# Kernel tuning notes

Hardware: AMD Instinct MI355X
Metric: run time of the kernel (lower is better)

## Reference

```python
import jax, jax.numpy as jnp
import numpy as np

# bitsandbytes NF4 codebook (16 levels)
NF4_CODE = jnp.array([
    -1.0, -0.6961928009986877, -0.5250730514526367, -0.39491748809814453,
    -0.28444138169288635, -0.18477343022823334, -0.09105003625154495, 0.0,
    0.07958029955625534, 0.16093020141124725, 0.24611230194568634,
    0.33791524171829224, 0.44070982933044434, 0.5626170039176941,
    0.7229568362236023, 1.0], dtype=jnp.float32)

L, D, KV, F, V = 2, 4096, 1024, 14336, 32000   # layers, d_model, kv_dim, ffn, vocab
H, HK, HD = 32, 8, 128                          # q heads, kv heads, head dim
B, S = 2, 1024
BLK = 64                                        # NF4 quant blocksize
ROPE_THETA = 500000.0
RMS_EPS = 1e-5


def _dequant(idx, absmax, shape):
    # idx: uint8 flat codes in [0,16); absmax: fp32 per-64-element block scale
    w = NF4_CODE[idx.astype(jnp.int32)]
    return (w.reshape(-1, BLK) * absmax[:, None]).reshape(shape)


def _rmsnorm(x, w):
    return x * jax.lax.rsqrt(jnp.mean(x * x, axis=-1, keepdims=True) + RMS_EPS) * w


def _rope(x, cos, sin):
    d2 = x.shape[-1] // 2
    x1, x2 = x[..., :d2], x[..., d2:]
    return jnp.concatenate([x1 * cos - x2 * sin, x2 * cos + x1 * sin], axis=-1)


def setup_inputs() -> dict:
    key = jax.random.key(0)
    ks = iter(jax.random.split(key, 64))

    def idx(n):
        return jax.random.randint(next(ks), (n,), 0, 16).astype(jnp.uint8)

    def amax(n):
        return jax.random.uniform(next(ks), (n // BLK,), minval=0.01, maxval=0.05)

    def qw(n):
        return (jnp.stack([idx(n) for _ in range(L)]),
                jnp.stack([amax(n) for _ in range(L)]))

    inp = {}
    inp["input_ids"] = jax.random.randint(next(ks), (B, S), 0, V, dtype=jnp.int32)
    inp["attention_mask"] = jnp.ones((B, S), dtype=jnp.int32)
    inp["embed"] = jax.random.normal(next(ks), (V, D), dtype=jnp.float32) * 0.02
    inp["q_idx"], inp["q_absmax"] = qw(D * D)
    inp["k_idx"], inp["k_absmax"] = qw(KV * D)
    inp["v_idx"], inp["v_absmax"] = qw(KV * D)
    inp["o_idx"], inp["o_absmax"] = qw(D * D)
    inp["gate_idx"], inp["gate_absmax"] = qw(F * D)
    inp["up_idx"], inp["up_absmax"] = qw(F * D)
    inp["down_idx"], inp["down_absmax"] = qw(D * F)
    inp["ln1_w"] = jnp.ones((L, D), dtype=jnp.float32)
    inp["ln2_w"] = jnp.ones((L, D), dtype=jnp.float32)
    inp["final_ln_w"] = jnp.ones((D,), dtype=jnp.float32)
    return inp


def reference(input_ids, attention_mask, embed,
              q_idx, q_absmax, k_idx, k_absmax, v_idx, v_absmax,
              o_idx, o_absmax, gate_idx, gate_absmax, up_idx, up_absmax,
              down_idx, down_absmax, ln1_w, ln2_w, final_ln_w):
    b, s = input_ids.shape
    h = embed[input_ids]                                  # [B,S,D]
    pos = jnp.arange(s, dtype=jnp.float32)
    inv = 1.0 / (ROPE_THETA ** (jnp.arange(0, HD, 2, dtype=jnp.float32) / HD))
    ang = pos[:, None] * inv[None, :]                     # [S,HD/2]
    cos = jnp.cos(ang)[None, :, None, :]
    sin = jnp.sin(ang)[None, :, None, :]
    causal = jnp.tril(jnp.ones((s, s), dtype=bool))
    mask = causal[None, None] & (attention_mask[:, None, None, :] > 0)  # [B,1,S,S]
    neg = jnp.finfo(h.dtype).min

    for l in range(L):
        x = _rmsnorm(h, ln1_w[l])
        q = x @ _dequant(q_idx[l], q_absmax[l], (D, D)).T
        k = x @ _dequant(k_idx[l], k_absmax[l], (KV, D)).T
        v = x @ _dequant(v_idx[l], v_absmax[l], (KV, D)).T
        q = _rope(q.reshape(b, s, H, HD), cos, sin)
        k = _rope(k.reshape(b, s, HK, HD), cos, sin)
        v = v.reshape(b, s, HK, HD)
        k = jnp.repeat(k, H // HK, axis=2)                # GQA expand
        v = jnp.repeat(v, H // HK, axis=2)
        scores = jnp.einsum('bqhd,bkhd->bhqk', q, k) / np.float32(np.sqrt(HD))
        scores = jnp.where(mask, scores, neg)
        attn = jax.nn.softmax(scores, axis=-1)
        ctx = jnp.einsum('bhqk,bkhd->bqhd', attn, v).reshape(b, s, D)
        h = h + ctx @ _dequant(o_idx[l], o_absmax[l], (D, D)).T
        x = _rmsnorm(h, ln2_w[l])
        g = x @ _dequant(gate_idx[l], gate_absmax[l], (F, D)).T
        u = x @ _dequant(up_idx[l], up_absmax[l], (F, D)).T
        h = h + (jax.nn.silu(g) * u) @ _dequant(down_idx[l], down_absmax[l], (D, F)).T

    h = _rmsnorm(h, final_ln_w)                           # last hidden state
    m = attention_mask.astype(h.dtype)[..., None]         # masked mean pool
    pooled = (h * m).sum(axis=1) / jnp.clip(m.sum(axis=1), 1e-9)
    return pooled
```

## Files before the change

kernel.cpp:

```cpp
#include <hip/hip_runtime.h>
#include <hip/hip_fp16.h>
#include <cstdint>
#include <cstddef>

#define B_  2
#define S_  1024
#define D_  4096
#define KV_ 1024
#define F_  14336
#define H_  32
#define HK_ 8
#define HD_ 128
#define M_  2048

typedef _Float16 f16;
typedef f16   f16x8 __attribute__((ext_vector_type(8)));
typedef f16   f16x4 __attribute__((ext_vector_type(4)));
typedef float f32x4 __attribute__((ext_vector_type(4)));

#define AS1(p) ((const __attribute__((address_space(1))) void*)(p))
#define AS3(p) ((__attribute__((address_space(3))) void*)(p))

__device__ __constant__ float NF4_C[16] = {
 -1.0f, -0.6961928009986877f, -0.5250730514526367f, -0.39491748809814453f,
 -0.28444138169288635f, -0.18477343022823334f, -0.09105003625154495f, 0.0f,
 0.07958029955625534f, 0.16093020141124725f, 0.24611230194568634f,
 0.33791524171829224f, 0.44070982933044434f, 0.5626170039176941f,
 0.7229568362236023f, 1.0f };

__global__ void k_detect(const unsigned* __restrict__ p, int* __restrict__ flag){
    if (threadIdx.x == 0){
        int u8 = 0;
        for (int i = 0; i < 256; ++i) if (p[i] >= 16u) { u8 = 1; break; }
        *flag = u8;
    }
}

__global__ __launch_bounds__(256) void k_dequant(const void* __restrict__ idxBase, size_t elemOff,
        const float* __restrict__ amax, f16* __restrict__ out, const int* __restrict__ flag)
{
    __shared__ __half2 T[3856];
    int t = threadIdx.x;
    if (t < 256){
        int b0 = t & 15, b1 = t >> 4;
        T[b0 + (b1 << 8)] = __halves2half2(__float2half(NF4_C[b0]), __float2half(NF4_C[b1]));
    }
    __syncthreads();
    size_t i = ((size_t)blockIdx.x * 256 + t) * 16;
    float am = amax[i >> 6];
    __half2 am2 = __float2half2_rn(am);
    union { __half2 h2[8]; uint4 u4[2]; } R;
    if (*flag){
        uint4 u = *(const uint4*)((const uint8_t*)idxBase + elemOff + i);
        unsigned w[4] = {u.x, u.y, u.z, u.w};
        #pragma unroll
        for (int j = 0; j < 4; ++j){
            R.h2[j*2+0] = __hmul2(T[w[j] & 0xFFFFu], am2);
            R.h2[j*2+1] = __hmul2(T[w[j] >> 16],     am2);
        }
    } else {
        const int4* s4 = (const int4*)((const int*)idxBase + elemOff + i);
        #pragma unroll
        for (int j = 0; j < 4; ++j){
            int4 a = s4[j];
            R.h2[j*2+0] = __hmul2(T[a.x | (a.y << 8)], am2);
            R.h2[j*2+1] = __hmul2(T[a.z | (a.w << 8)], am2);
        }
    }
    uint4* o = (uint4*)(out + i);
    o[0] = R.u4[0]; o[1] = R.u4[1];
}

__global__ __launch_bounds__(256) void k_embed(const int* __restrict__ ids,
        const float* __restrict__ E, float* __restrict__ Hh)
{
    int row = blockIdx.x, t = threadIdx.x;
    int id = ids[row];
    const float4* s4 = (const float4*)(E + (size_t)id * D_);
    float4* d4 = (float4*)(Hh + (size_t)row * D_);
    #pragma unroll
    for (int i = 0; i < 4; ++i) d4[t + 256*i] = s4[t + 256*i];
}

__global__ __launch_bounds__(256) void k_ropetab(float* __restrict__ cosT, float* __restrict__ sinT){
    int id = blockIdx.x * 256 + threadIdx.x;
    int d = id & 63, s = id >> 6;
    float inv = powf(500000.0f, -(float)d * (1.0f/64.0f));
    float ang = (float)s * inv;
    cosT[id] = cosf(ang);
    sinT[id] = sinf(ang);
}

__global__ void k_maskadd(const int* __restrict__ am, float* __restrict__ ma){
    int i = blockIdx.x * 256 + threadIdx.x;
    ma[i] = am[i] ? 0.f : -1e30f;
}

template<int F16OUT>
__global__ __launch_bounds__(256) void k_rmsnorm(const float* __restrict__ X,
        const float* __restrict__ W, void* __restrict__ outv)
{
    int row = blockIdx.x, t = threadIdx.x;
    const float4* x4 = (const float4*)(X + (size_t)row * D_);
    float4 xs[4]; float ss = 0.f;
    #pragma unroll
    for (int i = 0; i < 4; ++i){
        xs[i] = x4[t + 256*i];
        ss += xs[i].x*xs[i].x + xs[i].y*xs[i].y + xs[i].z*xs[i].z + xs[i].w*xs[i].w;
    }
    for (int m = 32; m; m >>= 1) ss += __shfl_xor(ss, m, 64);
    __shared__ float red[4];
    if ((t & 63) == 0) red[t >> 6] = ss;
    __syncthreads();
    ss = red[0] + red[1] + red[2] + red[3];
    float rs = rsqrtf(ss * (1.0f / D_) + 1e-5f);
    #pragma unroll
    for (int i = 0; i < 4; ++i){
        int c0 = (t + 256*i) * 4;
        float4 wv = *(const float4*)(W + c0);
        float o0 = xs[i].x*rs*wv.x, o1 = xs[i].y*rs*wv.y;
        float o2 = xs[i].z*rs*wv.z, o3 = xs[i].w*rs*wv.w;
        if (F16OUT){
            f16x4 ov = { (f16)o0, (f16)o1, (f16)o2, (f16)o3 };
            *(f16x4*)((f16*)outv + (size_t)row * D_ + c0) = ov;
        } else {
            float4 ov = {o0, o1, o2, o3};
            *(float4*)((float*)outv + (size_t)row * D_ + c0) = ov;
        }
    }
}

template<int LNH>
__global__ __launch_bounds__(256) void k_rope(const f16* __restrict__ in, int istr,
        f16* __restrict__ outp, const float* __restrict__ cosT, const float* __restrict__ sinT)
{
    int p = blockIdx.x * 256 + threadIdx.x;
    int d = p & 63;
    int h = (p >> 6) & ((1 << LNH) - 1);
    int s = (p >> (6 + LNH)) & (S_ - 1);
    int b = p >> (16 + LNH);
    size_t ib = (size_t)(b * S_ + s) * istr + (size_t)h * HD_;
    float x1 = (float)in[ib + d], x2 = (float)in[ib + 64 + d];
    float c = cosT[s*64 + d], sn = sinT[s*64 + d];
    size_t ob = (((size_t)((b << LNH) + h)) * S_ + (size_t)s) * HD_;
    outp[ob + d]      = (f16)(x1 * c - x2 * sn);
    outp[ob + 64 + d] = (f16)(x2 * c + x1 * sn);
}

__global__ __launch_bounds__(256) void k_vtrans(const f16* __restrict__ in, int istr,
        f16* __restrict__ outp){
    int p = blockIdx.x * 256 + threadIdx.x;
    int s  = p & (S_ - 1);
    int d  = (p >> 10) & (HD_ - 1);
    int hk = (p >> 17) & (HK_ - 1);
    int b  = p >> 20;
    f16 v = in[(size_t)(b * S_ + s) * istr + (size_t)hk * HD_ + d];
    outp[(((size_t)(b * HK_ + hk)) * HD_ + d) * S_ + s] = v;
}

__global__ __launch_bounds__(256) void k_flash(const f16* __restrict__ Qr, const f16* __restrict__ Kr,
        const f16* __restrict__ Vt, const float* __restrict__ mAddG, f16* __restrict__ ctx)
{
    __shared__ f16 KS[8192];
    __shared__ f16 VS[8192];
    __shared__ f16 PS[8192];
    const int t = threadIdx.x;
    const int w = t >> 6, l = t & 63;
    const int lr = l & 15, lg = l >> 4;
    const int qt = blockIdx.x, bh = blockIdx.y;
    const int b = bh >> 5, hh = bh & 31, hk = hh >> 2;
    const f16* Qb = Qr + ((size_t)bh * S_ + (size_t)qt*128) * HD_;
    const f16* Kb = Kr + (size_t)(b * HK_ + hk) * S_ * HD_;
    const f16* Vb = Vt + (size_t)(b * HK_ + hk) * HD_ * S_;

    auto stage16x128 = [&](const f16* src, int lds_, f16* dst){
        int rowl = t >> 4;
        int cs = ((t & 15) ^ (rowl & 7)) << 3;
        #pragma unroll
        for (int g = 0; g < 4; ++g)
            __builtin_amdgcn_global_load_lds(AS1(src + (size_t)(g*16 + rowl)*lds_ + cs),
                AS3(dst + g*2048 + w*512), 16, 0, 0);
    };
    auto stage32x64 = [&](const f16* src, int lds_, f16* dst){
        int rowl = t >> 3;
        int cs = ((t & 7) ^ (rowl & 7)) << 3;
        #pragma unroll
        for (int g = 0; g < 4; ++g)
            __builtin_amdgcn_global_load_lds(AS1(src + (size_t)(g*32 + rowl)*lds_ + cs),
                AS3(dst + g*2048 + w*512), 16, 0, 0);
    };

    stage16x128(Qb, HD_, KS);
    stage16x128(Qb + 64*HD_, HD_, VS);
    __syncthreads();
    f16x8 qF[2][4];
    {
        const f16* qsrc = (w < 2) ? KS : VS;
        int rbase = (w & 1) * 32;
        #pragma unroll
        for (int m = 0; m < 2; ++m)
            #pragma unroll
            for (int kd = 0; kd < 4; ++kd){
                int row = rbase + m*16 + lr;
                qF[m][kd] = *(const f16x8*)&qsrc[row*128 + (((kd*4 + lg) ^ (row & 7)) << 3)];
            }
    }
    __syncthreads();

    float mrow[2][4], lrow[2][4];
    f32x4 oacc[2][8];
    #pragma unroll
    for (int m = 0; m < 2; ++m)
        #pragma unroll
        for (int r = 0; r < 4; ++r){ mrow[m][r] = -1e30f; lrow[m][r] = 0.f; }
    #pragma unroll
    for (int m = 0; m < 2; ++m)
        #pragma unroll
        for (int dn = 0; dn < 8; ++dn){ f32x4 z = {0,0,0,0}; oacc[m][dn] = z; }

    const float ISQ = 0.08838834764831845f;
    const int ktMax = 2*qt + 1;

    for (int kt = 0; kt <= ktMax; ++kt){
        stage16x128(Kb + (size_t)(kt*64)*HD_, HD_, KS);
        __syncthreads();

        f32x4 sacc[2][4];
        #pragma unroll
        for (int m = 0; m < 2; ++m)
            #pragma unroll
            for (int n = 0; n < 4; ++n){ f32x4 z = {0,0,0,0}; sacc[m][n] = z; }
        #pragma unroll
        for (int n = 0; n < 4; ++n){
            int krow = n*16 + lr;
            #pragma unroll
            for (int kd = 0; kd < 4; ++kd){
                f16x8 kF = *(const f16x8*)&KS[krow*128 + (((kd*4 + lg) ^ (krow & 7)) << 3)];
                #pragma unroll
                for (int m = 0; m < 2; ++m)
                    sacc[m][n] = __builtin_amdgcn_mfma_f32_16x16x32_f16(qF[m][kd], kF, sacc[m][n], 0, 0, 0);
            }
        }

        stage32x64(Vb + kt*64, S_, VS);

        float mAdd[4];
        #pragma unroll
        for (int n = 0; n < 4; ++n) mAdd[n] = mAddG[b*S_ + kt*64 + n*16 + lr];
        int diag = (kt >= 2*qt);
        #pragma unroll
        for (int m = 0; m < 2; ++m)
        #pragma unroll
        for (int n = 0; n < 4; ++n)
        #pragma unroll
        for (int r = 0; r < 4; ++r){
            float s = sacc[m][n][r] * ISQ + mAdd[n];
            if (diag && (kt*64 + n*16 + lr) > (qt*128 + w*32 + m*16 + lg*4 + r)) s = -1e30f;
            sacc[m][n][r] = s;
        }
        #pragma unroll
        for (int m = 0; m < 2; ++m)
        #pragma unroll
        for (int r = 0; r < 4; ++r){
            float tm = fmaxf(fmaxf(sacc[m][0][r], sacc[m][1][r]), fmaxf(sacc[m][2][r], sacc[m][3][r]));
            #pragma unroll
            for (int msk = 1; msk < 16; msk <<= 1) tm = fmaxf(tm, __shfl_xor(tm, msk, 64));
            float mn = fmaxf(mrow[m][r], tm);
            float scl = __expf(mrow[m][r] - mn);
            mrow[m][r] = mn;
            float rs = 0.f;
            #pragma unroll
            for (int n = 0; n < 4; ++n){
                float p = __expf(sacc[m][n][r] - mn);
                sacc[m][n][r] = p; rs += p;
            }
            #pragma unroll
            for (int msk = 1; msk < 16; msk <<= 1) rs += __shfl_xor(rs, msk, 64);
            lrow[m][r] = lrow[m][r] * scl + rs;
            #pragma unroll
            for (int dn = 0; dn < 8; ++dn) oacc[m][dn][r] *= scl;
        }
        #pragma unroll
        for (int m = 0; m < 2; ++m)
        #pragma unroll
        for (int n = 0; n < 4; ++n)
        #pragma unroll
        for (int r = 0; r < 4; ++r){
            int rowl = m*16 + lg*4 + r;
            int slot = (n*2 + (lr >> 3)) ^ (rowl & 7);
            PS[w*2048 + rowl*64 + slot*8 + (lr & 7)] = (f16)sacc[m][n][r];
        }
        __syncthreads();

        f16x8 pF[2][2];
        #pragma unroll
        for (int m = 0; m < 2; ++m)
            #pragma unroll
            for (int kd = 0; kd < 2; ++kd){
                int prow = m*16 + lr;
                pF[m][kd] = *(const f16x8*)&PS[w*2048 + prow*64 + (((kd*4 + lg) ^ (prow & 7)) << 3)];
            }
        #pragma unroll
        for (int dn = 0; dn < 8; ++dn){
            int vrow = dn*16 + lr;
            #pragma unroll
            for (int kd = 0; kd < 2; ++kd){
                f16x8 vF = *(const f16x8*)&VS[vrow*64 + (((kd*4 + lg) ^ (vrow & 7)) << 3)];
                #pragma unroll
                for (int m = 0; m < 2; ++m)
                    oacc[m][dn] = __builtin_amdgcn_mfma_f32_16x16x32_f16(pF[m][kd], vF, oacc[m][dn], 0, 0, 0);
            }
        }
        __syncthreads();
    }

    #pragma unroll
    for (int m = 0; m < 2; ++m)
    #pragma unroll
    for (int dn = 0; dn < 8; ++dn)
    #pragma unroll
    for (int r = 0; r < 4; ++r){
        int grow = qt*128 + w*32 + m*16 + lg*4 + r;
        int gcol = hh*128 + dn*16 + lr;
        float v = oacc[m][dn][r] / fmaxf(lrow[m][r], 1e-30f);
        ctx[((size_t)(b * S_) + grow) * D_ + gcol] = (f16)v;
    }
}

template<int OUT>
__global__ __launch_bounds__(512, 1) void k_gemm3(const f16* __restrict__ A, const f16* __restrict__ Bp,
        void* __restrict__ Cv, const f16* __restrict__ G, int Kd, int ldk, int ldc)
{
    __shared__ f16 LDS[65536];
    const int t = threadIdx.x;
    const int w = t >> 6, l = t & 63;
    const int wm = w >> 2, wn = w & 3;

    int gx = gridDim.x, gy = gridDim.y;
    int nWG = gx * gy * gridDim.z;
    int n = (blockIdx.z * gy + blockIdx.y) * gx + blockIdx.x;
    int q = nWG >> 3;
    int sw = (n & 7) * q + (n >> 3);
    int bx = sw % gx; int r1 = sw / gx; int by = r1 % gy; int bz = r1 / gy;

    const int row0 = by * 256, col0 = bx * 256;
    const size_t koff = (size_t)bz * Kd;
    const int NT = Kd >> 6;

    const int swzk = ((t & 7) ^ ((t >> 3) & 7)) * 8;
    const f16* pA[2]; const f16* pB[2];
    #pragma unroll
    for (int l2 = 0; l2 < 2; ++l2){
        pA[l2] = A  + (size_t)(row0 + l2*128 + (t >> 3)) * ldk + koff + swzk;
        int wnc = (l2*64 + (t >> 3)) >> 5;
        pB[l2] = Bp + (size_t)(col0 + wnc*64 + ((t >> 3) & 31)) * ldk + koff + swzk;
    }

    auto stA = [&](int g, int tt, int buf){
        size_t so = (size_t)tt * 64;
        #pragma unroll
        for (int l2 = 0; l2 < 2; ++l2)
            __builtin_amdgcn_global_load_lds(AS1(pA[l2] + (size_t)g*64*ldk + so),
                AS3(&LDS[buf*16384 + g*8192 + l2*4096 + w*512]), 16, 0, 0);
    };
    auto stB = [&](int g, int tt, int buf){
        size_t so = (size_t)tt * 64;
        #pragma unroll
        for (int l2 = 0; l2 < 2; ++l2)
            __builtin_amdgcn_global_load_lds(AS1(pB[l2] + (size_t)g*32*ldk + so),
                AS3(&LDS[32768 + buf*16384 + g*8192 + l2*4096 + w*512]), 16, 0, 0);
    };

    const int lrow = (l & 15) * 64;
    const int kp0 = (((l >> 4))     ^ (l & 7)) * 8;
    const int kp1 = ((4 + (l >> 4)) ^ (l & 7)) * 8;

    f16x8 aR[2][4], bR0[2][2], bR1[2][2];
    auto rdA = [&](int g, int buf){
        int base = buf*16384 + g*8192 + wm*4096 + lrow;
        #pragma unroll
        for (int mf = 0; mf < 4; ++mf){
            aR[0][mf] = *(const f16x8*)&LDS[base + mf*1024 + kp0];
            aR[1][mf] = *(const f16x8*)&LDS[base + mf*1024 + kp1];
        }
    };
    auto rdB = [&](int g, int buf, f16x8 (&bR)[2][2]){
        int base = 32768 + buf*16384 + g*8192 + wn*2048 + lrow;
        #pragma unroll
        for (int nf = 0; nf < 2; ++nf){
            bR[0][nf] = *(const f16x8*)&LDS[base + nf*1024 + kp0];
            bR[1][nf] = *(const f16x8*)&LDS[base + nf*1024 + kp1];
        }
    };

    f32x4 zero = {0.f, 0.f, 0.f, 0.f};
    f32x4 acc[8][4];
    #pragma unroll
    for (int mi = 0; mi < 8; ++mi)
        #pragma unroll
        for (int ni = 0; ni < 4; ++ni) acc[mi][ni] = zero;

    #define MMQ(qm, qn, bR) { \
        __builtin_amdgcn_s_setprio(1); \
        _Pragma("unroll") \
        for (int ks = 0; ks < 2; ++ks) \
            _Pragma("unroll") \
            for (int mf = 0; mf < 4; ++mf) \
                _Pragma("unroll") \
                for (int nf = 0; nf < 2; ++nf) \
                    acc[(qm)*4+mf][(qn)*2+nf] = __builtin_amdgcn_mfma_f32_16x16x32_f16(aR[ks][mf], bR[ks][nf], acc[(qm)*4+mf][(qn)*2+nf], 0, 0, 0); \
        __builtin_amdgcn_s_setprio(0); }
    #define LGKM0 { asm volatile("s_waitcnt lgkmcnt(0)" ::: "memory"); __builtin_amdgcn_sched_barrier(0); }
    #define VM4   { asm volatile("s_waitcnt vmcnt(4)" ::: "memory"); }
    #define BAR   __builtin_amdgcn_s_barrier()

    stA(0, 0, 0); stB(1, 0, 0); stA(1, 0, 0); stB(0, 0, 0);
    if (NT > 1){ stA(0, 1, 1); stB(1, 1, 1); }
    VM4; BAR;

    for (int tt = 0; tt < NT; tt += 2){
        int c2 = (tt + 2 < NT) ? tt + 2 : NT - 1;
        int c3 = (tt + 3 < NT) ? tt + 3 : NT - 1;
        rdA(0, 0); rdB(0, 0, bR0);
        stA(1, tt+1 < NT ? tt+1 : NT-1, 1); stB(0, tt+1 < NT ? tt+1 : NT-1, 1);
        BAR; LGKM0; MMQ(0, 0, bR0); BAR;
        rdB(1, 0, bR1);
        BAR; LGKM0; MMQ(0, 1, bR1); BAR;
        rdA(1, 0);
        stA(0, c2, 0);
        BAR; LGKM0; MMQ(1, 1, bR1); BAR;
        stB(1, c2, 0);
        BAR; MMQ(1, 0, bR0); VM4; BAR;
        rdA(0, 1); rdB(0, 1, bR0);
        stA(1, c2, 0); stB(0, c2, 0);
        BAR; LGKM0; MMQ(0, 0, bR0); BAR;
        rdB(1, 1, bR1);
        BAR; LGKM0; MMQ(0, 1, bR1); BAR;
        rdA(1, 1);
        stA(0, c3, 1);
        BAR; LGKM0; MMQ(1, 1, bR1); BAR;
        stB(1, c3, 1);
        BAR; MMQ(1, 0, bR0); VM4; BAR;
    }

    #pragma unroll
    for (int mi = 0; mi < 8; ++mi)
    #pragma unroll
    for (int ni = 0; ni < 4; ++ni)
    #pragma unroll
    for (int r = 0; r < 4; ++r){
        int row = row0 + wm*128 + mi*16 + ((l >> 4) << 2) + r;
        int col = col0 + wn*64  + ni*16 + (l & 15);
        float v = acc[mi][ni][r];
        if (OUT == 0){
            ((float*)Cv)[(size_t)bz * ((size_t)M_ * ldc) + (size_t)row * ldc + col] = v;
        } else if (OUT == 2){
            ((f16*)Cv)[(size_t)row * ldc + col] = (f16)v;
        } else {
            size_t idx = (size_t)row * ldc + col;
            float g = (float)G[idx];
            float sg = g / (1.f + __expf(-g));
            ((f16*)Cv)[idx] = (f16)(sg * v);
        }
    }
    #undef MMQ
    #undef LGKM0
    #undef VM4
    #undef BAR
}

__global__ __launch_bounds__(256) void k_comb(const float* __restrict__ p0, const float* __restrict__ p1,
        float* __restrict__ outv)
{
    size_t i = ((size_t)blockIdx.x * 256 + threadIdx.x) * 4;
    float4 a = *(const float4*)(p0 + i);
    float4 b = *(const float4*)(p1 + i);
    float4 hv = *(const float4*)(outv + i);
    hv.x += a.x + b.x; hv.y += a.y + b.y; hv.z += a.z + b.z; hv.w += a.w + b.w;
    *(float4*)(outv + i) = hv;
}

__global__ __launch_bounds__(256) void k_pool1(const float* __restrict__ Hn, const int* __restrict__ amask,
        float* __restrict__ part, float* __restrict__ cntp)
{
    int d0 = blockIdx.x * 256 + threadIdx.x;
    int b  = blockIdx.y;
    int z  = blockIdx.z;
    int s0 = z * 128;
    float s = 0.f;
    for (int i = 0; i < 128; ++i){
        int row = s0 + i;
        if (amask[b * S_ + row])
            s += Hn[((size_t)(b * S_ + row)) * D_ + d0];
    }
    part[((size_t)(z * B_ + b)) * D_ + d0] = s;
    if (blockIdx.x == 0 && threadIdx.x == 0){
        float c = 0.f;
        for (int i = 0; i < 128; ++i) c += (amask[b * S_ + s0 + i] != 0) ? 1.f : 0.f;
        cntp[z * B_ + b] = c;
    }
}
__global__ __launch_bounds__(256) void k_pool2(const float* __restrict__ part, const float* __restrict__ cntp,
        float* __restrict__ outp)
{
    int gid = blockIdx.x * 256 + threadIdx.x;
    int b = gid >> 12, d = gid & (D_ - 1);
    float s = 0.f, c = 0.f;
    #pragma unroll
    for (int z = 0; z < 8; ++z){
        s += part[((size_t)(z * B_ + b)) * D_ + d];
        c += cntp[z * B_ + b];
    }
    outp[gid] = s / fmaxf(c, 1e-9f);
}

extern "C" void kernel_launch(void* const* d_in, const int* in_sizes, int n_in,
                              void* d_out, int out_size, void* d_ws, size_t ws_size,
                              hipStream_t stream)
{
    (void)in_sizes; (void)n_in; (void)out_size; (void)ws_size;
    const int*   ids   = (const int*)  d_in[0];
    const int*   amask = (const int*)  d_in[1];
    const float* embed = (const float*)d_in[2];
    const void*  qi = d_in[3];  const float* qa = (const float*)d_in[4];
    const void*  ki = d_in[5];  const float* ka = (const float*)d_in[6];
    const void*  vi = d_in[7];  const float* va = (const float*)d_in[8];
    const void*  oi = d_in[9];  const float* oa = (const float*)d_in[10];
    const void*  gi = d_in[11]; const float* ga = (const float*)d_in[12];
    const void*  ui = d_in[13]; const float* ua = (const float*)d_in[14];
    const void*  di = d_in[15]; const float* da = (const float*)d_in[16];
    const float* ln1 = (const float*)d_in[17];
    const float* ln2 = (const float*)d_in[18];
    const float* lnf = (const float*)d_in[19];

    const size_t DD  = (size_t)D_ * D_;
    const size_t KVD = (size_t)KV_ * D_;
    const size_t FD  = (size_t)F_ * D_;

    char* ws = (char*)d_ws;
    int*   flag = (int*)ws;
    float* h    = (float*)(ws + 256);
    float* cosT = (float*)(ws + 256 + 33554432);
    float* sinT = cosT + 65536;
    f16*   xin  = (f16*)(ws + 34078976);
    f16*   wbuf = (f16*)(ws + 50856192);
    char*  R4   = ws + 168296704;
    f16* qkv16 = (f16*)(R4);
    f16* qr  = (f16*)(R4 + 25165824);
    f16* kr  = (f16*)(R4 + 41943040);
    f16* vtr = (f16*)(R4 + 46137344);
    f16* ctx = (f16*)(R4 + 50331648);
    char* R5 = R4 + 67108864;
    f16*    gbuf   = (f16*)R5;
    float*  pR5_0  = (float*)R5;
    float*  pR5_1  = (float*)(R5 + 33554432);
    float*  pR4_0  = (float*)R4;
    float*  pR4_1  = (float*)(R4 + 33554432);
    float*  hn     = (float*)R4;
    float*  part   = (float*)R5;
    float*  cntp   = (float*)(R5 + 1048576);
    float*  maskAdd= (float*)(ws + 310378496);

    const int QKV_N = D_ + 2 * KV_;

    k_detect <<<1, 64, 0, stream>>>((const unsigned*)qi, flag);
    k_embed  <<<M_, 256, 0, stream>>>(ids, embed, h);
    k_ropetab<<<256, 256, 0, stream>>>(cosT, sinT);
    k_maskadd<<<(B_*S_)/256, 256, 0, stream>>>(amask, maskAdd);

    for (int l = 0; l < 2; ++l){
        size_t oDD = (size_t)l * DD, oKVD = (size_t)l * KVD, oFD = (size_t)l * FD;
        k_rmsnorm<1><<<M_, 256, 0, stream>>>(h, ln1 + l * D_, xin);

        k_dequant<<<DD / 4096, 256, 0, stream>>>(qi, oDD, qa + oDD/64, wbuf, flag);
        k_dequant<<<KVD / 4096, 256, 0, stream>>>(ki, oKVD, ka + oKVD/64, wbuf + DD, flag);
        k_dequant<<<KVD / 4096, 256, 0, stream>>>(vi, oKVD, va + oKVD/64, wbuf + DD + KVD, flag);
        k_gemm3<2><<<dim3(QKV_N/256, M_/256, 1), 512, 0, stream>>>(xin, wbuf, qkv16, nullptr, D_, D_, QKV_N);

        k_rope<5><<<(B_*S_*H_*64)/256, 256, 0, stream>>>(qkv16, QKV_N, qr, cosT, sinT);
        k_rope<3><<<(B_*S_*HK_*64)/256, 256, 0, stream>>>(qkv16 + D_, QKV_N, kr, cosT, sinT);
        k_vtrans <<<(B_*HK_*HD_*S_)/256, 256, 0, stream>>>(qkv16 + D_ + KV_, QKV_N, vtr);

        k_flash<<<dim3(S_/128, B_*H_), 256, 0, stream>>>(qr, kr, vtr, maskAdd, ctx);

        k_dequant<<<DD / 4096, 256, 0, stream>>>(oi, oDD, oa + oDD/64, wbuf, flag);
        k_gemm3<0><<<dim3(D_/256, M_/256, 2), 512, 0, stream>>>(ctx, wbuf, pR5_0, nullptr, D_/2, D_, D_);
        k_comb<<<(M_*D_)/1024, 256, 0, stream>>>(pR5_0, pR5_1, h);

        k_rmsnorm<1><<<M_, 256, 0, stream>>>(h, ln2 + l * D_, xin);
        k_dequant<<<FD / 4096, 256, 0, stream>>>(gi, oFD, ga + oFD/64, wbuf, flag);
        k_gemm3<2><<<dim3(F_/256, M_/256, 1), 512, 0, stream>>>(xin, wbuf, gbuf, nullptr, D_, D_, F_);
        k_dequant<<<FD / 4096, 256, 0, stream>>>(ui, oFD, ua + oFD/64, wbuf, flag);
        k_gemm3<3><<<dim3(F_/256, M_/256, 1), 512, 0, stream>>>(xin, wbuf, gbuf, gbuf, D_, D_, F_);
        k_dequant<<<FD / 4096, 256, 0, stream>>>(di, oFD, da + oFD/64, wbuf, flag);
        k_gemm3<0><<<dim3(D_/256, M_/256, 2), 512, 0, stream>>>(gbuf, wbuf, pR4_0, nullptr, F_/2, F_, D_);
        k_comb<<<(M_*D_)/1024, 256, 0, stream>>>(pR4_0, pR4_1, h);
    }

    k_rmsnorm<0><<<M_, 256, 0, stream>>>(h, lnf, hn);
    k_pool1<<<dim3(D_/256, B_, 8), 256, 0, stream>>>(hn, amask, part, cntp);
    k_pool2<<<(B_*D_)/256, 256, 0, stream>>>(part, cntp, (float*)d_out);
}
```

Before: 2.520 ms.

## Fuse NF4 dequantization into GEMM B-tile loads for o-proj and MLP

Adds k_gemm4, which reads the raw NF4 codes and absmax scales directly and dequantizes them through a half2 LUT into LDS while staging B tiles. It replaces the separate k_dequant pass plus fp16 weight buffer for the o, gate, up and down projections. This removes the round trip of writing and re-reading the dequantized weights through global memory. In exchange, B staging becomes synchronous register loads with VALU work in the pipelined loop instead of async global-to-LDS copies, and every row-tile block repeats the dequantization.

```diff
diff --git a/kernel.cpp b/kernel.cpp
--- a/kernel.cpp
+++ b/kernel.cpp
@@ -469,6 +469,179 @@
     #undef BAR
 }
 
+template<int OUT>
+__global__ __launch_bounds__(512, 1) void k_gemm4(const f16* __restrict__ A, const void* __restrict__ Bi,
+        size_t elemOff, const float* __restrict__ Ba, const int* __restrict__ flagp,
+        void* __restrict__ Cv, const f16* __restrict__ G, int Kd, int ldk, int ldc)
+{
+    __shared__ f16 LDS[65536];
+    __shared__ __half2 LUT[256];
+    const int t = threadIdx.x;
+    const int w = t >> 6, l = t & 63;
+    const int wm = w >> 2, wn = w & 3;
+
+    if (t < 256) LUT[t] = __halves2half2(__float2half(NF4_C[t & 15]), __float2half(NF4_C[t >> 4]));
+    const int isU8 = *flagp;
+
+    int gx = gridDim.x, gy = gridDim.y;
+    int nWG = gx * gy * gridDim.z;
+    int n = (blockIdx.z * gy + blockIdx.y) * gx + blockIdx.x;
+    int q = nWG >> 3;
+    int sw = (n & 7) * q + (n >> 3);
+    int bx = sw % gx; int r1 = sw / gx; int by = r1 % gy; int bz = r1 / gy;
+
+    const int row0 = by * 256, col0 = bx * 256;
+    const size_t koff = (size_t)bz * Kd;
+    const int NT = Kd >> 6;
+    const int kb = ldk >> 6;
+
+    const int swzk = ((t & 7) ^ ((t >> 3) & 7)) * 8;
+    const f16* pA[2];
+    size_t eBs[2], aBs[2];
+    #pragma unroll
+    for (int l2 = 0; l2 < 2; ++l2){
+        pA[l2] = A  + (size_t)(row0 + l2*128 + (t >> 3)) * ldk + koff + swzk;
+        int wnc = (l2*64 + (t >> 3)) >> 5;
+        int rowB = col0 + wnc*64 + ((t >> 3) & 31);
+        eBs[l2] = elemOff + (size_t)rowB * ldk + koff + swzk;
+        aBs[l2] = ((size_t)rowB * ldk + koff) >> 6;
+    }
+    const uint8_t* Bu8 = (const uint8_t*)Bi;
+    const int*     Bi32 = (const int*)Bi;
+
+    auto stA = [&](int g, int tt, int buf){
+        size_t so = (size_t)tt * 64;
+        #pragma unroll
+        for (int l2 = 0; l2 < 2; ++l2)
+            __builtin_amdgcn_global_load_lds(AS1(pA[l2] + (size_t)g*64*ldk + so),
+                AS3(&LDS[buf*16384 + g*8192 + l2*4096 + w*512]), 16, 0, 0);
+    };
+    auto stB4 = [&](int g, int tt, int buf){
+        #pragma unroll
+        for (int l2 = 0; l2 < 2; ++l2){
+            size_t eoff = eBs[l2] + (size_t)g*32*ldk + (size_t)tt*64;
+            float am = Ba[aBs[l2] + (size_t)g*32*kb + tt];
+            __half2 am2 = __float2half2_rn(am);
+            union { __half2 h2[4]; f16x8 v; } R;
+            if (isU8){
+                uint2 u = *(const uint2*)(Bu8 + eoff);
+                unsigned x0 = u.x & 0xFFFFu, x1 = u.x >> 16, x2 = u.y & 0xFFFFu, x3 = u.y >> 16;
+                R.h2[0] = __hmul2(LUT[(x0 | (x0 >> 4)) & 0xFF], am2);
+                R.h2[1] = __hmul2(LUT[(x1 | (x1 >> 4)) & 0xFF], am2);
+                R.h2[2] = __hmul2(LUT[(x2 | (x2 >> 4)) & 0xFF], am2);
+                R.h2[3] = __hmul2(LUT[(x3 | (x3 >> 4)) & 0xFF], am2);
+            } else {
+                int4 a0 = *(const int4*)(Bi32 + eoff);
+                int4 a1 = *(const int4*)(Bi32 + eoff + 4);
+                R.h2[0] = __hmul2(LUT[a0.x | (a0.y << 4)], am2);
+                R.h2[1] = __hmul2(LUT[a0.z | (a0.w << 4)], am2);
+                R.h2[2] = __hmul2(LUT[a1.x | (a1.y << 4)], am2);
+                R.h2[3] = __hmul2(LUT[a1.z | (a1.w << 4)], am2);
+            }
+            *(f16x8*)&LDS[32768 + buf*16384 + g*8192 + l2*4096 + w*512 + l*8] = R.v;
+        }
+    };
+
+    const int lrow = (l & 15) * 64;
+    const int kp0 = (((l >> 4))     ^ (l & 7)) * 8;
+    const int kp1 = ((4 + (l >> 4)) ^ (l & 7)) * 8;
+
+    f16x8 aR[2][4], bR0[2][2], bR1[2][2];
+    auto rdA = [&](int g, int buf){
+        int base = buf*16384 + g*8192 + wm*4096 + lrow;
+        #pragma unroll
+        for (int mf = 0; mf < 4; ++mf){
+            aR[0][mf] = *(const f16x8*)&LDS[base + mf*1024 + kp0];
+            aR[1][mf] = *(const f16x8*)&LDS[base + mf*1024 + kp1];
+        }
+    };
+    auto rdB = [&](int g, int buf, f16x8 (&bR)[2][2]){
+        int base = 32768 + buf*16384 + g*8192 + wn*2048 + lrow;
+        #pragma unroll
+        for (int nf = 0; nf < 2; ++nf){
+            bR[0][nf] = *(const f16x8*)&LDS[base + nf*1024 + kp0];
+            bR[1][nf] = *(const f16x8*)&LDS[base + nf*1024 + kp1];
+        }
+    };
+
+    f32x4 zero = {0.f, 0.f, 0.f, 0.f};
+    f32x4 acc[8][4];
+    #pragma unroll
+    for (int mi = 0; mi < 8; ++mi)
+        #pragma unroll
+        for (int ni = 0; ni < 4; ++ni) acc[mi][ni] = zero;
+
+    #define MMQ(qm, qn, bR) { \
+        __builtin_amdgcn_s_setprio(1); \
+        _Pragma("unroll") \
+        for (int ks = 0; ks < 2; ++ks) \
+            _Pragma("unroll") \
+            for (int mf = 0; mf < 4; ++mf) \
+                _Pragma("unroll") \
+                for (int nf = 0; nf < 2; ++nf) \
+                    acc[(qm)*4+mf][(qn)*2+nf] = __builtin_amdgcn_mfma_f32_16x16x32_f16(aR[ks][mf], bR[ks][nf], acc[(qm)*4+mf][(qn)*2+nf], 0, 0, 0); \
+        __builtin_amdgcn_s_setprio(0); }
+    #define LGKM0 { asm volatile("s_waitcnt lgkmcnt(0)" ::: "memory"); __builtin_amdgcn_sched_barrier(0); }
+    #define VM2   { asm volatile("s_waitcnt vmcnt(2)" ::: "memory"); }
+    #define BAR   __builtin_amdgcn_s_barrier()
+
+    __syncthreads();
+    stA(0, 0, 0); stA(1, 0, 0);
+    stB4(1, 0, 0); stB4(0, 0, 0);
+    if (NT > 1){ stA(0, 1, 1); stB4(1, 1, 1); }
+    VM2; BAR;
+
+    for (int tt = 0; tt < NT; tt += 2){
+        int c2 = (tt + 2 < NT) ? tt + 2 : NT - 1;
+        int c3 = (tt + 3 < NT) ? tt + 3 : NT - 1;
+        rdA(0, 0); rdB(0, 0, bR0);
+        stA(1, tt+1 < NT ? tt+1 : NT-1, 1); stB4(0, tt+1 < NT ? tt+1 : NT-1, 1);
+        BAR; LGKM0; MMQ(0, 0, bR0); BAR;
+        rdB(1, 0, bR1);
+        BAR; LGKM0; MMQ(0, 1, bR1); BAR;
+        rdA(1, 0);
+        stA(0, c2, 0);
+        BAR; LGKM0; MMQ(1, 1, bR1); BAR;
+        stB4(1, c2, 0);
+        BAR; MMQ(1, 0, bR0); VM2; BAR;
+        rdA(0, 1); rdB(0, 1, bR0);
+        stA(1, c2, 0); stB4(0, c2, 0);
+        BAR; LGKM0; MMQ(0, 0, bR0); BAR;
+        rdB(1, 1, bR1);
+        BAR; LGKM0; MMQ(0, 1, bR1); BAR;
+        rdA(1, 1);
+        stA(0, c3, 1);
+        BAR; LGKM0; MMQ(1, 1, bR1); BAR;
+        stB4(1, c3, 1);
+        BAR; MMQ(1, 0, bR0); VM2; BAR;
+    }
+
+    #pragma unroll
+    for (int mi = 0; mi < 8; ++mi)
+    #pragma unroll
+    for (int ni = 0; ni < 4; ++ni)
+    #pragma unroll
+    for (int r = 0; r < 4; ++r){
+        int row = row0 + wm*128 + mi*16 + ((l >> 4) << 2) + r;
+        int col = col0 + wn*64  + ni*16 + (l & 15);
+        float v = acc[mi][ni][r];
+        if (OUT == 0){
+            ((float*)Cv)[(size_t)bz * ((size_t)M_ * ldc) + (size_t)row * ldc + col] = v;
+        } else if (OUT == 2){
+            ((f16*)Cv)[(size_t)row * ldc + col] = (f16)v;
+        } else {
+            size_t idx = (size_t)row * ldc + col;
+            float g = (float)G[idx];
+            float sg = g / (1.f + __expf(-g));
+            ((f16*)Cv)[idx] = (f16)(sg * v);
+        }
+    }
+    #undef MMQ
+    #undef LGKM0
+    #undef VM2
+    #undef BAR
+}
+
 __global__ __launch_bounds__(256) void k_comb(const float* __restrict__ p0, const float* __restrict__ p1,
         float* __restrict__ outv)
 {
@@ -583,17 +756,17 @@
 
         k_flash<<<dim3(S_/128, B_*H_), 256, 0, stream>>>(qr, kr, vtr, maskAdd, ctx);
 
-        k_dequant<<<DD / 4096, 256, 0, stream>>>(oi, oDD, oa + oDD/64, wbuf, flag);
-        k_gemm3<0><<<dim3(D_/256, M_/256, 2), 512, 0, stream>>>(ctx, wbuf, pR5_0, nullptr, D_/2, D_, D_);
+        k_gemm4<0><<<dim3(D_/256, M_/256, 2), 512, 0, stream>>>(ctx, oi, oDD, oa + oDD/64, flag,
+            pR5_0, nullptr, D_/2, D_, D_);
         k_comb<<<(M_*D_)/1024, 256, 0, stream>>>(pR5_0, pR5_1, h);
 
         k_rmsnorm<1><<<M_, 256, 0, stream>>>(h, ln2 + l * D_, xin);
-        k_dequant<<<FD / 4096, 256, 0, stream>>>(gi, oFD, ga + oFD/64, wbuf, flag);
-        k_gemm3<2><<<dim3(F_/256, M_/256, 1), 512, 0, stream>>>(xin, wbuf, gbuf, nullptr, D_, D_, F_);
-        k_dequant<<<FD / 4096, 256, 0, stream>>>(ui, oFD, ua + oFD/64, wbuf, flag);
-        k_gemm3<3><<<dim3(F_/256, M_/256, 1), 512, 0, stream>>>(xin, wbuf, gbuf, gbuf, D_, D_, F_);
-        k_dequant<<<FD / 4096, 256, 0, stream>>>(di, oFD, da + oFD/64, wbuf, flag);
-        k_gemm3<0><<<dim3(D_/256, M_/256, 2), 512, 0, stream>>>(gbuf, wbuf, pR4_0, nullptr, F_/2, F_, D_);
+        k_gemm4<2><<<dim3(F_/256, M_/256, 1), 512, 0, stream>>>(xin, gi, oFD, ga + oFD/64, flag,
+            gbuf, nullptr, D_, D_, F_);
+        k_gemm4<3><<<dim3(F_/256, M_/256, 1), 512, 0, stream>>>(xin, ui, oFD, ua + oFD/64, flag,
+            gbuf, gbuf, D_, D_, F_);
+        k_gemm4<0><<<dim3(D_/256, M_/256, 2), 512, 0, stream>>>(gbuf, di, oFD, da + oFD/64, flag,
+            pR4_0, nullptr, F_/2, F_, D_);
         k_comb<<<(M_*D_)/1024, 256, 0, stream>>>(pR4_0, pR4_1, h);
     }
 
```

After: 4.981 ms. 97.7% more time.
